# Optimization experiments

Hardware: AMD Instinct MI355X
Metric: run time of the kernel (lower is better)

The kernel has to match this reference:

```python
import jax, jax.numpy as jnp
import numpy as np

B, T, C = 128, 512, 512
EPS = 1e-5


def setup_inputs() -> dict:
    key = jax.random.key(0)
    ks = jax.random.split(key, 12)
    s_tri = 1.0 / np.sqrt(T)   # rough torch Linear init scale (per-row fan-in varies; fixed for simplicity)
    s_fc1 = 1.0 / np.sqrt(C)
    s_fc2 = 1.0 / np.sqrt(2 * C)
    return {
        "inputs": jax.random.normal(ks[0], (B, T, C), dtype=jnp.float32),
        "ln1_w": jnp.ones((T, C), jnp.float32),
        "ln1_b": jnp.zeros((T, C), jnp.float32),
        "ln2_w": jnp.ones((T, C), jnp.float32),
        "ln2_b": jnp.zeros((T, C), jnp.float32),
        # Row s of triu_W corresponds to nn.Linear(s+1, 1); entries j> s are masked in reference().
        "triu_W": jax.random.uniform(ks[1], (T, T), jnp.float32, -s_tri, s_tri),
        "triu_b": jax.random.uniform(ks[2], (T,), jnp.float32, -s_tri, s_tri),
        "fc1_W": jax.random.uniform(ks[3], (2 * C, C), jnp.float32, -s_fc1, s_fc1),
        "fc1_b": jax.random.uniform(ks[4], (2 * C,), jnp.float32, -s_fc1, s_fc1),
        "fc2_W": jax.random.uniform(ks[5], (C, 2 * C), jnp.float32, -s_fc2, s_fc2),
        "fc2_b": jax.random.uniform(ks[6], (C,), jnp.float32, -s_fc2, s_fc2),
    }


def _layernorm_2d(x, w, b):
    # torch nn.LayerNorm((T, C)): normalize jointly over the last TWO dims.
    mu = jnp.mean(x, axis=(-2, -1), keepdims=True)
    var = jnp.var(x, axis=(-2, -1), keepdims=True)
    return (x - mu) * jax.lax.rsqrt(var + EPS) * w + b


def reference(inputs, ln1_w, ln1_b, ln2_w, ln2_b, triu_W, triu_b, fc1_W, fc1_b, fc2_W, fc2_b):
    x = _layernorm_2d(inputs, ln1_w, ln1_b)                       # [B,T,C]
    # TriU time mixer on x.mT ([B,C,T]): out[..., s] = sum_{t<=s} W[s,t]*x[..., t] + b[s]
    Wm = jnp.tril(triu_W)                                          # causal mask
    xm = jnp.einsum('btc,st->bsc', x, Wm) + triu_b[None, :, None]  # [B,T,C] (already back-transposed)
    x2 = _layernorm_2d(xm + inputs, ln2_w, ln2_b)                  # [B,T,C]
    h = jax.nn.gelu(jnp.einsum('btc,hc->bth', x2, fc1_W) + fc1_b, approximate=False)
    y = jnp.einsum('bth,ch->btc', h, fc2_W) + fc2_b
    return x2 + y
```

## Files before the change

kernel.cpp:

```cpp
#include <hip/hip_runtime.h>
#include <hip/hip_fp8.h>
#include <cstdint>

typedef unsigned short u16;
typedef unsigned char u8;
typedef __attribute__((ext_vector_type(8))) short s16x8;
typedef __attribute__((ext_vector_type(4))) float f32x4;
typedef __attribute__((ext_vector_type(8))) unsigned short u16x8;
typedef __attribute__((ext_vector_type(4))) unsigned short u16x4;
typedef __attribute__((ext_vector_type(4))) unsigned char u8x4;
typedef __attribute__((ext_vector_type(8))) unsigned char u8x8;

#define B_ 128
#define T_ 512
#define C_ 512
#define TC 262144

static __device__ __forceinline__ float bf2f(u16 u) {
  union { unsigned int i; float f; } v; v.i = ((unsigned int)u) << 16; return v.f;
}
static __device__ __forceinline__ u16 f2bf(float f) {
  union { float fv; unsigned int i; } v; v.fv = f;
  unsigned int r = (v.i + 0x7FFFu + ((v.i >> 16) & 1u)) >> 16;
  return (u16)r;
}
static __device__ __forceinline__ u8 f2fp8(float f) {
  __hip_fp8_e4m3 v(f);
  return *(u8*)&v;
}

static __device__ __forceinline__ float gelu_fast(float x) {
  float x2 = x * x;
  float arg = 1.5957691216057308f * x * fmaf(0.044715f, x2, 1.0f);
  return x / (1.0f + __expf(-arg));
}

#define GLD16(gp, lp) __builtin_amdgcn_global_load_lds( \
    (const __attribute__((address_space(1))) void*)(gp), \
    (__attribute__((address_space(3))) void*)(lp), 16, 0, 0)


__global__ __launch_bounds__(256)
void reduce_stats_kernel(const float* __restrict__ X, float2* __restrict__ partials,
                         u16* __restrict__ Xb,
                         const float* __restrict__ triu_W, u16* __restrict__ wmb,
                         const float* __restrict__ fc1_W, u8* __restrict__ w1f8,
                         const float* __restrict__ fc2_W, u8* __restrict__ w2f8) {
  const int b = blockIdx.y, blk = blockIdx.x, tid = threadIdx.x;
  const size_t gi = (size_t)b * TC + (size_t)blk * 2048 + (size_t)tid * 8;
  const float* p = X + gi;
  f32x4 v0 = *(const f32x4*)p;
  f32x4 v1 = *(const f32x4*)(p + 4);
  float s = 0.f, q = 0.f;
  u16x8 ob;
#pragma unroll
  for (int i = 0; i < 4; ++i) {
    s += v0[i] + v1[i]; q += v0[i] * v0[i] + v1[i] * v1[i];
    ob[i] = f2bf(v0[i]); ob[4 + i] = f2bf(v1[i]);
  }
  *(u16x8*)(Xb + gi) = ob;

  const int flat = (b * 128 + blk) * 256 + tid;
  if (flat < T_ * T_) {
    const int sr = flat >> 9, tcol = flat & 511;
    wmb[flat] = f2bf(tcol <= sr ? triu_W[flat] : 0.f);
  }
  if (flat < 2 * C_ * C_) {
    w1f8[flat] = f2fp8(fc1_W[flat]);
    w2f8[flat] = f2fp8(fc2_W[flat]);
  }

  for (int o = 32; o; o >>= 1) { s += __shfl_down(s, o); q += __shfl_down(q, o); }
  __shared__ float ss[4], qq[4];
  if ((tid & 63) == 0) { ss[tid >> 6] = s; qq[tid >> 6] = q; }
  __syncthreads();
  if (tid == 0)
    partials[(size_t)b * 128 + blk] =
        make_float2(ss[0] + ss[1] + ss[2] + ss[3], qq[0] + qq[1] + qq[2] + qq[3]);
}


__global__ __launch_bounds__(256)
void ln1_transpose_kernel(const u16* __restrict__ Xb, const float* __restrict__ W,
                          const float* __restrict__ Bv, const float2* __restrict__ partials,
                          u16* __restrict__ xT) {
  const int b = blockIdx.z;
  const int t0 = blockIdx.y * 64, c0 = blockIdx.x * 64;
  const int tid = threadIdx.x;
  __shared__ u16 tile[64][72];
  __shared__ float smu, srs;

  if (tid < 64) {
    float2 p0 = partials[(size_t)b * 128 + tid];
    float2 p1 = partials[(size_t)b * 128 + 64 + tid];
    float s = p0.x + p1.x, q = p0.y + p1.y;
    for (int o = 32; o; o >>= 1) { s += __shfl_down(s, o); q += __shfl_down(q, o); }
    if (tid == 0) {
      float mean = s * (1.f / (float)TC);
      float var = q * (1.f / (float)TC) - mean * mean;
      smu = mean; srs = rsqrtf(var + 1e-5f);
    }
  }
  __syncthreads();
  const float mu = smu, rs = srs;

  const int rr = tid >> 4;
  const int cc = (tid & 15) * 4;
#pragma unroll
  for (int i = 0; i < 4; ++i) {
    const int lt = i * 16 + rr;
    const size_t wi = (size_t)(t0 + lt) * C_ + c0 + cc;
    u16x4 xa = *(const u16x4*)(Xb + (size_t)b * TC + wi);
    f32x4 w = *(const f32x4*)(W + wi);
    f32x4 bb = *(const f32x4*)(Bv + wi);
#pragma unroll
    for (int j = 0; j < 4; ++j)
      tile[lt][cc + j] = f2bf((bf2f(xa[j]) - mu) * rs * w[j] + bb[j]);
  }
  __syncthreads();
  const int c = tid >> 2;
  const int tg = (tid & 3) * 16;
  u16 buf[16];
#pragma unroll
  for (int i = 0; i < 16; ++i) buf[i] = tile[tg + i][c];
  const size_t o = (size_t)b * TC + (size_t)(c0 + c) * T_ + t0 + tg;
  u16x8 o0, o1;
#pragma unroll
  for (int i = 0; i < 8; ++i) { o0[i] = buf[i]; o1[i] = buf[8 + i]; }
  *(u16x8*)(xT + o) = o0;
  *(u16x8*)(xT + o + 8) = o1;
}


__global__ __launch_bounds__(256)
void ln2_apply_kernel(const u16* __restrict__ S, const float* __restrict__ W,
                      const float* __restrict__ Bv, const float2* __restrict__ partials2,
                      u16* __restrict__ x2, u8* __restrict__ x8) {
  const size_t i = ((size_t)blockIdx.x * 256 + threadIdx.x) * 8;
  const int b = (int)(i >> 18);
  const size_t r = i & (size_t)(TC - 1);
  float2 p0 = partials2[(size_t)b * 4 + 0];
  float2 p1 = partials2[(size_t)b * 4 + 1];
  float2 p2 = partials2[(size_t)b * 4 + 2];
  float2 p3 = partials2[(size_t)b * 4 + 3];
  float s = (p0.x + p1.x) + (p2.x + p3.x);
  float q = (p0.y + p1.y) + (p2.y + p3.y);
  const float mu = s * (1.f / (float)TC);
  const float rs = rsqrtf(q * (1.f / (float)TC) - mu * mu + 1e-5f);

  u16x8 sv = *(const u16x8*)(S + i);
  f32x4 w0 = *(const f32x4*)(W + r);
  f32x4 w1 = *(const f32x4*)(W + r + 4);
  f32x4 b0 = *(const f32x4*)(Bv + r);
  f32x4 b1 = *(const f32x4*)(Bv + r + 4);
  u16x8 o;
  u8x8 o8;
#pragma unroll
  for (int j = 0; j < 4; ++j) {
    float v0 = (bf2f(sv[j])     - mu) * rs * w0[j] + b0[j];
    float v1 = (bf2f(sv[4 + j]) - mu) * rs * w1[j] + b1[j];
    o[j] = f2bf(v0); o[4 + j] = f2bf(v1);
    o8[j] = f2fp8(v0); o8[4 + j] = f2fp8(v1);
  }
  *(u16x8*)(x2 + i) = o;
  *(u8x8*)(x8 + i) = o8;
}


template <int MODE>
__global__ __launch_bounds__(512, (MODE == 0) ? 1 : 2)
void gemm_bt_kernel(const u16* __restrict__ A, const u16* __restrict__ Bm,
                    int K, int lda, int ldb,
                    void* __restrict__ Cp, int ldc,
                    const float* __restrict__ bias,
                    const void* __restrict__ res,
                    long long strideB, long long strideC,
                    float2* __restrict__ stat_part) {
  constexpr int TILE_U16 = (MODE == 0) ? 16384 : 8192;
  __shared__ u16 Asb[2 * TILE_U16];
  __shared__ u16 Bsb[2 * TILE_U16];
  __shared__ float rs_[8], rq_[8];
  const int tid = threadIdx.x;

  const int nwg = gridDim.x;
  const int orig = blockIdx.x;
  const int swz = (orig & 7) * (nwg >> 3) + (orig >> 3);
  int bx, by, bz;
  if (MODE == 0) { bz = swz >> 2; by = (swz >> 1) & 1; bx = swz & 1; }
  else if (MODE == 1) { bz = 0; by = swz >> 2; bx = swz & 3; }
  else { bz = 0; by = swz >> 1; bx = swz & 1; }

  const u16* Bp = Bm + (size_t)bz * (size_t)strideB;
  const int m0 = by * 256, n0 = bx * 256;
  int kTiles = K >> 6;
  if (MODE == 0) { const int need = (by + 1) * 4; if (need < kTiles) kTiles = need; }

  const int lane = tid & 63;
  const int wave = tid >> 6;
  const int wm = (wave >> 2) * 128;
  const int wn = (wave & 3) * 64;
  const int lr = lane & 15;
  const int kg = lane >> 4;

  f32x4 acc[8][4];
  const f32x4 zero = {0.f, 0.f, 0.f, 0.f};
#pragma unroll
  for (int m = 0; m < 8; ++m)
#pragma unroll
    for (int n = 0; n < 4; ++n) acc[m][n] = zero;

  auto STAGE_A = [&](int t) {
    const int k0 = t << 6;
    const int d = (t & 1) * 16384;
#pragma unroll
    for (int p = 0; p < 4; ++p) {
      const int q = p * 512 + tid;
      const int r = q >> 3;
      const int kcs = (q & 7) ^ (r & 7);
      GLD16(A + (size_t)(m0 + r) * lda + k0 + (kcs << 3), &Asb[d + q * 8]);
    }
  };
  auto STAGE_B = [&](int t) {
    const int k0 = t << 6;
    const int d = (t & 1) * 16384;
#pragma unroll
    for (int p = 0; p < 4; ++p) {
      const int q = p * 512 + tid;
      const int r = q >> 3;
      const int kcs = (q & 7) ^ (r & 7);
      GLD16(Bp + (size_t)(n0 + r) * ldb + k0 + (kcs << 3), &Bsb[d + q * 8]);
    }
  };
  auto STAGE_A8 = [&](int t) {
    const int k0 = t << 6;
    u8* lds = (u8*)Asb + (t & 1) * 16384;
    const u8* src = (const u8*)A;
#pragma unroll
    for (int p = 0; p < 2; ++p) {
      const int q = p * 512 + tid;
      const int r = q >> 2;
      const int c16 = (q & 3) ^ ((r >> 2) & 3);
      GLD16(src + (size_t)(m0 + r) * lda + k0 + c16 * 16, lds + q * 16);
    }
  };
  auto STAGE_B8 = [&](int t) {
    const int k0 = t << 6;
    u8* lds = (u8*)Bsb + (t & 1) * 16384;
    const u8* src = (const u8*)Bp;
#pragma unroll
    for (int p = 0; p < 2; ++p) {
      const int q = p * 512 + tid;
      const int r = q >> 2;
      const int c16 = (q & 3) ^ ((r >> 2) & 3);
      GLD16(src + (size_t)(n0 + r) * ldb + k0 + c16 * 16, lds + q * 16);
    }
  };

  if (MODE == 0) {
    STAGE_A(0); STAGE_B(0); STAGE_A(1);
    for (int kt = 0; kt < kTiles; ++kt) {
      const int d = (kt & 1) * 16384;
      if (kt + 1 < kTiles) asm volatile("s_waitcnt vmcnt(4)" ::: "memory");
      else                 asm volatile("s_waitcnt vmcnt(0)" ::: "memory");
      __builtin_amdgcn_s_barrier();
      asm volatile("" ::: "memory");

      s16x8 a0[8], a1[8], b0[4], b1[4];
#pragma unroll
      for (int m = 0; m < 8; ++m) {
        const int row = wm + m * 16 + lr;
        const u16* base = &Asb[d + row * 64];
        a0[m] = *(const s16x8*)(base + (((kg)     ^ (row & 7)) << 3));
        a1[m] = *(const s16x8*)(base + (((4 + kg) ^ (row & 7)) << 3));
      }
#pragma unroll
      for (int n = 0; n < 4; ++n) {
        const int row = wn + n * 16 + lr;
        b0[n] = *(const s16x8*)(&Bsb[d + row * 64] + (((kg) ^ (row & 7)) << 3));
      }
      if (kt + 1 < kTiles) STAGE_B(kt + 1);

      __builtin_amdgcn_s_setprio(1);
#pragma unroll
      for (int m = 0; m < 8; ++m)
#pragma unroll
        for (int n = 0; n < 4; ++n)
          acc[m][n] = __builtin_amdgcn_mfma_f32_16x16x32_bf16(a0[m], b0[n], acc[m][n], 0, 0, 0);
      __builtin_amdgcn_s_setprio(0);

#pragma unroll
      for (int n = 0; n < 4; ++n) {
        const int row = wn + n * 16 + lr;
        b1[n] = *(const s16x8*)(&Bsb[d + row * 64] + (((4 + kg) ^ (row & 7)) << 3));
      }
      asm volatile("s_waitcnt lgkmcnt(0)" ::: "memory");
      __builtin_amdgcn_s_barrier();
      asm volatile("" ::: "memory");
      if (kt + 2 < kTiles) STAGE_A(kt + 2);

      __builtin_amdgcn_s_setprio(1);
#pragma unroll
      for (int m = 0; m < 8; ++m)
#pragma unroll
        for (int n = 0; n < 4; ++n)
          acc[m][n] = __builtin_amdgcn_mfma_f32_16x16x32_bf16(a1[m], b1[n], acc[m][n], 0, 0, 0);
      __builtin_amdgcn_s_setprio(0);
    }
  } else {
    STAGE_A8(0); STAGE_B8(0); STAGE_A8(1);
    for (int kt = 0; kt < kTiles; ++kt) {
      const u8* Ad = (const u8*)Asb + (kt & 1) * 16384;
      const u8* Bd = (const u8*)Bsb + (kt & 1) * 16384;
      if (kt + 1 < kTiles) asm volatile("s_waitcnt vmcnt(2)" ::: "memory");
      else                 asm volatile("s_waitcnt vmcnt(0)" ::: "memory");
      __builtin_amdgcn_s_barrier();
      asm volatile("" ::: "memory");

      long a0[8], a1[8], b0[4], b1[4];
      const int sub = (kg & 1) * 8;
      const int hi = kg >> 1;
#pragma unroll
      for (int m = 0; m < 8; ++m) {
        const int row = wm + m * 16 + lr;
        const u8* base = Ad + row * 64;
        const int sw = (row >> 2) & 3;
        a0[m] = *(const long*)(base + ((hi)     ^ sw) * 16 + sub);
        a1[m] = *(const long*)(base + ((2 + hi) ^ sw) * 16 + sub);
      }
#pragma unroll
      for (int n = 0; n < 4; ++n) {
        const int row = wn + n * 16 + lr;
        const int sw = (row >> 2) & 3;
        b0[n] = *(const long*)(Bd + row * 64 + ((hi) ^ sw) * 16 + sub);
      }
      if (kt + 1 < kTiles) STAGE_B8(kt + 1);

      __builtin_amdgcn_s_setprio(1);
#pragma unroll
      for (int m = 0; m < 8; ++m)
#pragma unroll
        for (int n = 0; n < 4; ++n)
          acc[m][n] = __builtin_amdgcn_mfma_f32_16x16x32_fp8_fp8(a0[m], b0[n], acc[m][n], 0, 0, 0);
      __builtin_amdgcn_s_setprio(0);

#pragma unroll
      for (int n = 0; n < 4; ++n) {
        const int row = wn + n * 16 + lr;
        const int sw = (row >> 2) & 3;
        b1[n] = *(const long*)(Bd + row * 64 + ((2 + hi) ^ sw) * 16 + sub);
      }
      asm volatile("s_waitcnt lgkmcnt(0)" ::: "memory");
      __builtin_amdgcn_s_barrier();
      asm volatile("" ::: "memory");
      if (kt + 2 < kTiles) STAGE_A8(kt + 2);

      __builtin_amdgcn_s_setprio(1);
#pragma unroll
      for (int m = 0; m < 8; ++m)
#pragma unroll
        for (int n = 0; n < 4; ++n)
          acc[m][n] = __builtin_amdgcn_mfma_f32_16x16x32_fp8_fp8(a1[m], b1[n], acc[m][n], 0, 0, 0);
      __builtin_amdgcn_s_setprio(0);
    }
  }

  if (MODE == 0) {
    u16* Cptr = (u16*)Cp + (size_t)bz * (size_t)strideC;
    const u16* inp = (const u16*)res + (size_t)bz * (size_t)strideC;
    float psum = 0.f, psq = 0.f;
#pragma unroll
    for (int m = 0; m < 8; ++m) {
      const int rb = m0 + wm + m * 16 + kg * 4;
#pragma unroll
      for (int n = 0; n < 4; ++n) {
        const int col = n0 + wn + n * 16 + lr;
#pragma unroll
        for (int j = 0; j < 4; ++j) {
          const size_t idx = (size_t)(rb + j) * ldc + col;
          float v = acc[m][n][j] + bf2f(inp[idx]) + bias[rb + j];
          psum += v; psq += v * v;
          Cptr[idx] = f2bf(v);
        }
      }
    }
    for (int o = 32; o; o >>= 1) { psum += __shfl_down(psum, o); psq += __shfl_down(psq, o); }
    if (lane == 0) { rs_[wave] = psum; rq_[wave] = psq; }
    __syncthreads();
    if (tid == 0) {
      float s = 0.f, q = 0.f;
#pragma unroll
      for (int w = 0; w < 8; ++w) { s += rs_[w]; q += rq_[w]; }
      stat_part[(size_t)bz * 4 + by * 2 + bx] = make_float2(s, q);
    }
  } else if (MODE == 1) {
    u8* Cptr = (u8*)Cp;
#pragma unroll
    for (int m = 0; m < 8; ++m) {
      const int rb = m0 + wm + m * 16 + kg * 4;
#pragma unroll
      for (int n = 0; n < 4; ++n) {
        const int col = n0 + wn + n * 16 + lr;
        const float bs = bias[col];
#pragma unroll
        for (int j = 0; j < 4; ++j) {
          float v = acc[m][n][j] + bs;
          Cptr[(size_t)(rb + j) * ldc + col] = f2fp8(gelu_fast(v));
        }
      }
    }
  } else {
    float* Cptr = (float*)Cp;
    const u16* x2p = (const u16*)res;
#pragma unroll
    for (int m = 0; m < 8; ++m) {
      const int rb = m0 + wm + m * 16 + kg * 4;
#pragma unroll
      for (int n = 0; n < 4; ++n) {
        const int col = n0 + wn + n * 16 + lr;
        const float bs = bias[col];
#pragma unroll
        for (int j = 0; j < 4; ++j) {
          const size_t idx = (size_t)(rb + j) * ldc + col;
          Cptr[idx] = acc[m][n][j] + bs + bf2f(x2p[idx]);
        }
      }
    }
  }
}


extern "C" void kernel_launch(void* const* d_in, const int* in_sizes, int n_in,
                              void* d_out, int out_size, void* d_ws, size_t ws_size,
                              hipStream_t stream) {
  const float* inputs = (const float*)d_in[0];
  const float* ln1_w  = (const float*)d_in[1];
  const float* ln1_b  = (const float*)d_in[2];
  const float* ln2_w  = (const float*)d_in[3];
  const float* ln2_b  = (const float*)d_in[4];
  const float* triu_W = (const float*)d_in[5];
  const float* triu_b = (const float*)d_in[6];
  const float* fc1_W  = (const float*)d_in[7];
  const float* fc1_b  = (const float*)d_in[8];
  const float* fc2_W  = (const float*)d_in[9];
  const float* fc2_b  = (const float*)d_in[10];
  float* out = (float*)d_out;
  (void)in_sizes; (void)n_in; (void)out_size; (void)ws_size;

  char* ws = (char*)d_ws;
  size_t off = 0;
  auto carve = [&](size_t bytes) {
    char* p = ws + off;
    off += (bytes + 255) & ~(size_t)255;
    return p;
  };
  u16* s_bf = (u16*)carve((size_t)B_ * T_ * C_ * 2);
  u16* xT   = (u16*)carve((size_t)B_ * T_ * C_ * 2);
  u16* x2   = xT;
  u16* inb  = (u16*)carve((size_t)B_ * T_ * C_ * 2);
  u8*  x8   = (u8*)carve((size_t)B_ * T_ * C_);
  u8*  h    = (u8*)carve((size_t)B_ * T_ * 2 * C_);
  u16* wmb  = (u16*)carve((size_t)T_ * T_ * 2);
  u8*  w1f8 = (u8*)carve((size_t)2 * C_ * C_);
  u8*  w2f8 = (u8*)carve((size_t)C_ * 2 * C_);
  float2* partials  = (float2*)carve(128 * 128 * sizeof(float2));
  float2* partials2 = (float2*)carve(128 * 4 * sizeof(float2));

  reduce_stats_kernel<<<dim3(128, 128), 256, 0, stream>>>(
      inputs, partials, inb, triu_W, wmb, fc1_W, w1f8, fc2_W, w2f8);
  ln1_transpose_kernel<<<dim3(8, 8, 128), 256, 0, stream>>>(inb, ln1_w, ln1_b, partials, xT);
  gemm_bt_kernel<0><<<512, 512, 0, stream>>>(
      wmb, xT, 512, 512, 512, s_bf, 512, triu_b, inb, (long long)TC, (long long)TC, partials2);
  ln2_apply_kernel<<<16384, 256, 0, stream>>>(s_bf, ln2_w, ln2_b, partials2, x2, x8);
  gemm_bt_kernel<1><<<1024, 512, 0, stream>>>(
      (const u16*)x8, (const u16*)w1f8, 512, 512, 512, h, 1024, fc1_b, nullptr, 0, 0, nullptr);
  gemm_bt_kernel<2><<<512, 512, 0, stream>>>(
      (const u16*)h, (const u16*)w2f8, 1024, 1024, 1024, out, 512, fc2_b, x2, 0, 0, nullptr);
}
```

Before: 355.2 us.

## Use packed hardware FP8 conversion and re-swizzle FP8 GEMM LDS tiles to 128-byte rows

```diff
diff --git a/kernel.cpp b/kernel.cpp
--- a/kernel.cpp
+++ b/kernel.cpp
@@ -8,8 +8,6 @@
 typedef __attribute__((ext_vector_type(4))) float f32x4;
 typedef __attribute__((ext_vector_type(8))) unsigned short u16x8;
 typedef __attribute__((ext_vector_type(4))) unsigned short u16x4;
-typedef __attribute__((ext_vector_type(4))) unsigned char u8x4;
-typedef __attribute__((ext_vector_type(8))) unsigned char u8x8;
 
 #define B_ 128
 #define T_ 512
@@ -24,9 +22,10 @@
   unsigned int r = (v.i + 0x7FFFu + ((v.i >> 16) & 1u)) >> 16;
   return (u16)r;
 }
-static __device__ __forceinline__ u8 f2fp8(float f) {
-  __hip_fp8_e4m3 v(f);
-  return *(u8*)&v;
+static __device__ __forceinline__ unsigned int cvtpk_fp8(float a, float b) {
+  unsigned int r;
+  asm volatile("v_cvt_pk_fp8_f32 %0, %1, %2" : "=v"(r) : "v"(a), "v"(b));
+  return r & 0xffffu;
 }
 
 static __device__ __forceinline__ float gelu_fast(float x) {
@@ -65,9 +64,11 @@
     const int sr = flat >> 9, tcol = flat & 511;
     wmb[flat] = f2bf(tcol <= sr ? triu_W[flat] : 0.f);
   }
-  if (flat < 2 * C_ * C_) {
-    w1f8[flat] = f2fp8(fc1_W[flat]);
-    w2f8[flat] = f2fp8(fc2_W[flat]);
+  if (flat < C_ * C_) {
+    float2 a1 = *(const float2*)(fc1_W + (size_t)flat * 2);
+    float2 a2 = *(const float2*)(fc2_W + (size_t)flat * 2);
+    *(u16*)(w1f8 + (size_t)flat * 2) = (u16)cvtpk_fp8(a1.x, a1.y);
+    *(u16*)(w2f8 + (size_t)flat * 2) = (u16)cvtpk_fp8(a2.x, a2.y);
   }
 
   for (int o = 32; o; o >>= 1) { s += __shfl_down(s, o); q += __shfl_down(q, o); }
@@ -154,16 +155,18 @@
   f32x4 b0 = *(const f32x4*)(Bv + r);
   f32x4 b1 = *(const f32x4*)(Bv + r + 4);
   u16x8 o;
-  u8x8 o8;
+  float v[8];
 #pragma unroll
   for (int j = 0; j < 4; ++j) {
-    float v0 = (bf2f(sv[j])     - mu) * rs * w0[j] + b0[j];
-    float v1 = (bf2f(sv[4 + j]) - mu) * rs * w1[j] + b1[j];
-    o[j] = f2bf(v0); o[4 + j] = f2bf(v1);
-    o8[j] = f2fp8(v0); o8[4 + j] = f2fp8(v1);
+    v[j]     = (bf2f(sv[j])     - mu) * rs * w0[j] + b0[j];
+    v[4 + j] = (bf2f(sv[4 + j]) - mu) * rs * w1[j] + b1[j];
+    o[j] = f2bf(v[j]); o[4 + j] = f2bf(v[4 + j]);
   }
   *(u16x8*)(x2 + i) = o;
-  *(u8x8*)(x8 + i) = o8;
+  uint2 pk;
+  pk.x = cvtpk_fp8(v[0], v[1]) | (cvtpk_fp8(v[2], v[3]) << 16);
+  pk.y = cvtpk_fp8(v[4], v[5]) | (cvtpk_fp8(v[6], v[7]) << 16);
+  *(uint2*)(x8 + i) = pk;
 }
 
 
@@ -238,9 +241,10 @@
 #pragma unroll
     for (int p = 0; p < 2; ++p) {
       const int q = p * 512 + tid;
-      const int r = q >> 2;
-      const int c16 = (q & 3) ^ ((r >> 2) & 3);
-      GLD16(src + (size_t)(m0 + r) * lda + k0 + c16 * 16, lds + q * 16);
+      const int lrow = q >> 3;
+      const int cp = (q & 7) ^ (lrow & 7);
+      const int dr = lrow + ((cp & 4) << 5);
+      GLD16(src + (size_t)(m0 + dr) * lda + k0 + ((cp & 3) << 4), lds + q * 16);
     }
   };
   auto STAGE_B8 = [&](int t) {
@@ -250,9 +254,10 @@
 #pragma unroll
     for (int p = 0; p < 2; ++p) {
       const int q = p * 512 + tid;
-      const int r = q >> 2;
-      const int c16 = (q & 3) ^ ((r >> 2) & 3);
-      GLD16(src + (size_t)(n0 + r) * ldb + k0 + c16 * 16, lds + q * 16);
+      const int lrow = q >> 3;
+      const int cp = (q & 7) ^ (lrow & 7);
+      const int dr = lrow + ((cp & 4) << 5);
+      GLD16(src + (size_t)(n0 + dr) * ldb + k0 + ((cp & 3) << 4), lds + q * 16);
     }
   };
 
@@ -321,17 +326,19 @@
       const int hi = kg >> 1;
 #pragma unroll
       for (int m = 0; m < 8; ++m) {
-        const int row = wm + m * 16 + lr;
-        const u8* base = Ad + row * 64;
-        const int sw = (row >> 2) & 3;
-        a0[m] = *(const long*)(base + ((hi)     ^ sw) * 16 + sub);
-        a1[m] = *(const long*)(base + ((2 + hi) ^ sw) * 16 + sub);
-      }
-#pragma unroll
-      for (int n = 0; n < 4; ++n) {
-        const int row = wn + n * 16 + lr;
-        const int sw = (row >> 2) & 3;
-        b0[n] = *(const long*)(Bd + row * 64 + ((hi) ^ sw) * 16 + sub);
+        const int dd = wm + m * 16 + lr;
+        const int lrow = dd & 127;
+        const int g4 = (dd >> 7) << 2;
+        const u8* base = Ad + lrow * 128 + sub;
+        a0[m] = *(const long*)(base + (((g4 | hi)       ^ (lrow & 7)) << 4));
+        a1[m] = *(const long*)(base + (((g4 | (2 + hi)) ^ (lrow & 7)) << 4));
+      }
+#pragma unroll
+      for (int n = 0; n < 4; ++n) {
+        const int dd = wn + n * 16 + lr;
+        const int lrow = dd & 127;
+        const int g4 = (dd >> 7) << 2;
+        b0[n] = *(const long*)(Bd + lrow * 128 + sub + (((g4 | hi) ^ (lrow & 7)) << 4));
       }
       if (kt + 1 < kTiles) STAGE_B8(kt + 1);
 
@@ -345,9 +352,10 @@
 
 #pragma unroll
       for (int n = 0; n < 4; ++n) {
-        const int row = wn + n * 16 + lr;
-        const int sw = (row >> 2) & 3;
-        b1[n] = *(const long*)(Bd + row * 64 + ((2 + hi) ^ sw) * 16 + sub);
+        const int dd = wn + n * 16 + lr;
+        const int lrow = dd & 127;
+        const int g4 = (dd >> 7) << 2;
+        b1[n] = *(const long*)(Bd + lrow * 128 + sub + (((g4 | (2 + hi)) ^ (lrow & 7)) << 4));
       }
       asm volatile("s_waitcnt lgkmcnt(0)" ::: "memory");
       __builtin_amdgcn_s_barrier();
@@ -401,11 +409,14 @@
       for (int n = 0; n < 4; ++n) {
         const int col = n0 + wn + n * 16 + lr;
         const float bs = bias[col];
-#pragma unroll
-        for (int j = 0; j < 4; ++j) {
-          float v = acc[m][n][j] + bs;
-          Cptr[(size_t)(rb + j) * ldc + col] = f2fp8(gelu_fast(v));
-        }
+        unsigned int p01 = cvtpk_fp8(gelu_fast(acc[m][n][0] + bs),
+                                     gelu_fast(acc[m][n][1] + bs));
+        unsigned int p23 = cvtpk_fp8(gelu_fast(acc[m][n][2] + bs),
+                                     gelu_fast(acc[m][n][3] + bs));
+        Cptr[(size_t)(rb + 0) * ldc + col] = (u8)(p01 & 0xff);
+        Cptr[(size_t)(rb + 1) * ldc + col] = (u8)(p01 >> 8);
+        Cptr[(size_t)(rb + 2) * ldc + col] = (u8)(p23 & 0xff);
+        Cptr[(size_t)(rb + 3) * ldc + col] = (u8)(p23 >> 8);
       }
     }
   } else {
```

Result: no change. 353.3 us (-0.5%).
